# Performance work log

Hardware: AMD Instinct MI355X
Metric: run time of the kernel (lower is better)

Reference implementation:

```python
import jax, jax.numpy as jnp
import numpy as np

TEMPERATURE = 2.0


def _offdiag_idx(n):
    # flat indices of the off-diagonal entries of an [n, n] matrix, row-major,
    # reshaped to [n, n-1] (matches torch masked_select(~eye).view(n, n-1))
    idx = np.arange(n * n).reshape(n, n)
    return jnp.asarray(idx[~np.eye(n, dtype=bool)].reshape(n, n - 1))


def setup_inputs() -> dict:
    key = jax.random.key(0)
    k1, k2, k3, k4 = jax.random.split(key, 4)
    B, D = 256, 512
    return {
        "wt_emb": jax.random.normal(k1, (B, D), dtype=jnp.float32),
        "mt_emb": jax.random.normal(k2, (B, D), dtype=jnp.float32),
        "label_wt": jax.random.uniform(k3, (B,), dtype=jnp.float32),
        "label_mt": jax.random.uniform(k4, (B,), dtype=jnp.float32),
    }


def reference(wt_emb, mt_emb, label_wt, label_mt):
    t = TEMPERATURE
    features = jnp.concatenate([wt_emb, mt_emb], axis=0)            # [n, D]
    labels = jnp.concatenate([label_wt, label_mt], axis=0)[:, None]  # [n, 1]
    n = features.shape[0]

    # L1 label differences: [n, n]
    label_diffs = jnp.abs(labels[:, None, :] - labels[None, :, :]).sum(-1)

    # negative L2 feature distances (safe sqrt: diagonal is exactly 0)
    diff = features[:, None, :] - features[None, :, :]               # [n, n, D]
    sq = jnp.sum(diff * diff, axis=-1)                               # [n, n]
    dist = jnp.where(sq > 0, jnp.sqrt(jnp.where(sq > 0, sq, 1.0)), 0.0)
    logits = -dist / t
    logits = logits - jax.lax.stop_gradient(jnp.max(logits, axis=1, keepdims=True))
    exp_logits = jnp.exp(logits)

    # drop diagonal -> [n, n-1]
    off = _offdiag_idx(n)
    lo = logits.reshape(-1)[off]
    eo = exp_logits.reshape(-1)[off]
    ldo = label_diffs.reshape(-1)[off]

    # vectorized over positive index k: mask[i, k, j] = ld[i, j] >= ld[i, k]
    neg_mask = ldo[:, None, :] >= ldo[:, :, None]                    # [n, n-1, n-1]
    denom = jnp.sum(jnp.where(neg_mask, eo[:, None, :], 0.0), axis=-1)  # [n, n-1]
    pos_log_probs = lo - jnp.log(denom)                              # [n, n-1]
    return -jnp.sum(pos_log_probs) / (n * (n - 1))
```

## Files before the change

### kernel.cpp

```cpp
#include <hip/hip_runtime.h>


#define N 512
#define B 256
#define D 512
#define NT 512
#define NBLK (N / 2)

#define WS_SL    0
#define WS_NORM  512
#define WS_PART  1024
#define WS_FH    2048

typedef _Float16 half4_t  __attribute__((ext_vector_type(4)));
typedef _Float16 half8_t  __attribute__((ext_vector_type(8)));
typedef float    f32x4    __attribute__((ext_vector_type(4)));

__global__ __launch_bounds__(NT) void sort_rows_kernel(
    const float* __restrict__ wt, const float* __restrict__ mt,
    const float* __restrict__ lwt, const float* __restrict__ lmt,
    float* __restrict__ ws)
{
    const int t = threadIdx.x, b = blockIdx.x;
    __shared__ float slab[N];
    __shared__ int scnt[4];
    __shared__ float swred[NT / 64];
    slab[t] = (t < B) ? lwt[t] : lmt[t - B];
    if (t < 4) scnt[t] = 0;
    __syncthreads();

    const int jj = t >> 7, j = b * 4 + jj;
    const int c = t & 127;
    const float lj = slab[j];
    int r = 0;
    #pragma unroll
    for (int x = c * 4; x < c * 4 + 4; ++x) {
        const float v = slab[x];
        r += (v < lj || (v == lj && x < j)) ? 1 : 0;
    }
    #pragma unroll
    for (int off = 32; off > 0; off >>= 1)
        r += __shfl_down(r, off, 64);
    if ((t & 63) == 0) atomicAdd(&scnt[jj], r);
    __syncthreads();

    if (t < 4)
        ws[WS_SL + scnt[t]] = slab[b * 4 + t];

    const int rr = scnt[jj];
    const float* F = (j < B) ? (wt + (size_t)j * D) : (mt + (size_t)(j - B) * D);
    const float4 v = ((const float4*)F)[c];
    half4_t h;
    h[0] = (_Float16)v.x; h[1] = (_Float16)v.y;
    h[2] = (_Float16)v.z; h[3] = (_Float16)v.w;
    ((half4_t*)((_Float16*)(ws + WS_FH) + (size_t)rr * D))[c] = h;
    const float f0 = (float)h[0], f1 = (float)h[1];
    const float f2 = (float)h[2], f3 = (float)h[3];
    float nacc = f0 * f0 + f1 * f1 + f2 * f2 + f3 * f3;
    #pragma unroll
    for (int off = 32; off > 0; off >>= 1)
        nacc += __shfl_down(nacc, off, 64);
    if ((t & 63) == 0) swred[t >> 6] = nacc;
    __syncthreads();
    if (t < 4)
        ws[WS_NORM + scnt[t]] = swred[2 * t] + swred[2 * t + 1];
}

__global__ __launch_bounds__(NT) void rnc_main(float* __restrict__ ws)
{
    const int b = blockIdx.x, i0 = 2 * b, i1 = 2 * b + 1;
    const int t = threadIdx.x;
    const int w = t >> 6, lane = t & 63;

    __shared__ float sl[N];
    __shared__ float snm[N];
    __shared__ __align__(16) float sp0[N];
    __shared__ __align__(16) float sf0[N];
    __shared__ __align__(16) float sp1[N];
    __shared__ __align__(16) float sf1[N];
    __shared__ float sg0[N];
    __shared__ float sg1[N];
    __shared__ float sred[NT / 64];

    sl[t]  = ws[WS_SL + t];
    snm[t] = ws[WS_NORM + t];

    const _Float16* Fh = (const _Float16*)(ws + WS_FH);
    const int quad = lane >> 4, m = lane & 15;
    const _Float16* Ap = Fh + (size_t)(i0 + (m & 1)) * D + quad * 8;
    const _Float16* Bp[4];
    #pragma unroll
    for (int u = 0; u < 4; ++u)
        Bp[u] = Fh + (size_t)((w * 4 + u) * 16 + m) * D + quad * 8;

    f32x4 acc[4] = {{0.f,0.f,0.f,0.f},{0.f,0.f,0.f,0.f},
                    {0.f,0.f,0.f,0.f},{0.f,0.f,0.f,0.f}};
    #pragma unroll
    for (int k0 = 0; k0 < D; k0 += 32) {
        const half8_t a = *(const half8_t*)(Ap + k0);
        #pragma unroll
        for (int u = 0; u < 4; ++u) {
            const half8_t bb = *(const half8_t*)(Bp[u] + k0);
            acc[u] = __builtin_amdgcn_mfma_f32_16x16x32_f16(a, bb, acc[u], 0, 0, 0);
        }
    }
    if (quad == 0) {
        #pragma unroll
        for (int u = 0; u < 4; ++u) {
            const int col = w * 64 + u * 16 + m;
            sg0[col] = acc[u][0];
            sg1[col] = acc[u][1];
        }
    }
    __syncthreads();

    const float li0 = sl[i0], li1 = sl[i1];
    const float ni0 = snm[i0], ni1 = snm[i1];

    const float g0 = sg0[t];
    const float g1 = sg1[t];
    const float d0 = fmaxf(ni0 + snm[t] - 2.f * g0, 0.f);
    const float d1 = fmaxf(ni1 + snm[t] - 2.f * g1, 0.f);
    const float lg0 = -0.5f * sqrtf(d0);
    const float lg1 = -0.5f * sqrtf(d1);
    float lg_acc = 0.f;
    if (t != i0) lg_acc += lg0;
    if (t != i1) lg_acc += lg1;
    const float e0 = (t == i0) ? 0.f : __expf(lg0);
    const float e1 = (t == i1) ? 0.f : __expf(lg1);
    sp0[t] = e0; sf0[t] = e0;
    sp1[t] = e1; sf1[t] = e1;
    __syncthreads();

    if (w < 4) {
        float* arr = (w == 0) ? sp0 : (w == 1) ? sf0 : (w == 2) ? sp1 : sf1;
        float4* a4 = (float4*)arr;
        float4 u0 = a4[lane * 2], u1 = a4[lane * 2 + 1];
        float v0 = u0.x, v1 = u0.y, v2 = u0.z, v3 = u0.w;
        float v4 = u1.x, v5 = u1.y, v6 = u1.z, v7 = u1.w;
        if ((w & 1) == 0) {
            v1 += v0; v2 += v1; v3 += v2; v4 += v3; v5 += v4; v6 += v5; v7 += v6;
            float x = v7;
            #pragma unroll
            for (int off = 1; off < 64; off <<= 1) {
                const float y = __shfl_up(x, off, 64);
                if (lane >= off) x += y;
            }
            float ex = __shfl_up(x, 1, 64);
            if (lane == 0) ex = 0.f;
            v0 += ex; v1 += ex; v2 += ex; v3 += ex; v4 += ex; v5 += ex; v6 += ex; v7 += ex;
        } else {
            v6 += v7; v5 += v6; v4 += v5; v3 += v4; v2 += v3; v1 += v2; v0 += v1;
            float x = v0;
            #pragma unroll
            for (int off = 1; off < 64; off <<= 1) {
                const float y = __shfl_down(x, off, 64);
                if (lane + off < 64) x += y;
            }
            float ex = __shfl_down(x, 1, 64);
            if (lane == 63) ex = 0.f;
            v0 += ex; v1 += ex; v2 += ex; v3 += ex; v4 += ex; v5 += ex; v6 += ex; v7 += ex;
        }
        a4[lane * 2]     = make_float4(v0, v1, v2, v3);
        a4[lane * 2 + 1] = make_float4(v4, v5, v6, v7);
    }
    __syncthreads();

    float local = lg_acc;
    #pragma unroll
    for (int p = 0; p < 2; ++p) {
        const int x = t;
        const int ri = p ? i1 : i0;
        const float li = p ? li1 : li0;
        const float* SP = p ? sp1 : sp0;
        const float* SF = p ? sf1 : sf0;
        if (x != ri) {
            const float th = fabsf(li - sl[x]);
            int lo = 0, hi = ri + 1;
            while (lo < hi) {
                const int mid = (lo + hi) >> 1;
                if (fabsf(li - sl[mid]) >= th) lo = mid + 1; else hi = mid;
            }
            const int a = lo;
            lo = ri + 1; hi = N;
            while (lo < hi) {
                const int mid = (lo + hi) >> 1;
                if (fabsf(li - sl[mid]) >= th) hi = mid; else lo = mid + 1;
            }
            const int bb = lo;
            const float denom = ((a > 0) ? SP[a - 1] : 0.f) + ((bb < N) ? SF[bb] : 0.f);
            local -= __logf(denom);
        }
    }

    #pragma unroll
    for (int off = 32; off > 0; off >>= 1)
        local += __shfl_down(local, off, 64);
    if (lane == 0) sred[w] = local;
    __syncthreads();
    if (t == 0) {
        float sum = 0.f;
        #pragma unroll
        for (int k = 0; k < NT / 64; ++k) sum += sred[k];
        ws[WS_PART + b] = sum;
    }
}

__global__ __launch_bounds__(NBLK) void rnc_finalize(
    const float* __restrict__ ws, float* __restrict__ out)
{
    const int t = threadIdx.x;
    __shared__ float sred[NBLK / 64];
    float v = ws[WS_PART + t];
    #pragma unroll
    for (int off = 32; off > 0; off >>= 1)
        v += __shfl_down(v, off, 64);
    if ((t & 63) == 0) sred[t >> 6] = v;
    __syncthreads();
    if (t == 0) {
        float sum = 0.f;
        #pragma unroll
        for (int k = 0; k < NBLK / 64; ++k) sum += sred[k];
        out[0] = -sum / (float)((long)N * (N - 1));
    }
}

extern "C" void kernel_launch(void* const* d_in, const int* in_sizes, int n_in,
                              void* d_out, int out_size, void* d_ws, size_t ws_size,
                              hipStream_t stream) {
    const float* wt  = (const float*)d_in[0];
    const float* mt  = (const float*)d_in[1];
    const float* lwt = (const float*)d_in[2];
    const float* lmt = (const float*)d_in[3];
    float* out = (float*)d_out;
    float* ws  = (float*)d_ws;

    sort_rows_kernel<<<128, NT, 0, stream>>>(wt, mt, lwt, lmt, ws);
    rnc_main<<<NBLK, NT, 0, stream>>>(ws);
    rnc_finalize<<<1, NBLK, 0, stream>>>(ws, out);
}
```

Baseline: 83.37 us.

## Compute full Gram matrix in a separate MFMA kernel instead of per-block

Moves the feature Gram computation out of the per-row-pair main kernel into a dedicated kernel that computes the full 512x512 matrix with 32x32 MFMA tiles per wave and writes it to workspace. The main kernel now just loads its two Gram rows. This removes the heavy redundancy where every block streamed the full fp16 feature matrix and issued MFMAs using only two output rows per tile. It adds an extra kernel launch and a round trip of the Gram matrix through global memory.

```diff
diff --git a/kernel.cpp b/kernel.cpp
--- a/kernel.cpp
+++ b/kernel.cpp
@@ -11,6 +11,7 @@
 #define WS_NORM  512
 #define WS_PART  1024
 #define WS_FH    2048
+#define WS_G     (2048 + (N * D) / 2)
 
 typedef _Float16 half4_t  __attribute__((ext_vector_type(4)));
 typedef _Float16 half8_t  __attribute__((ext_vector_type(8)));
@@ -66,6 +67,46 @@
         ws[WS_NORM + scnt[t]] = swred[2 * t] + swred[2 * t + 1];
 }
 
+__global__ __launch_bounds__(256) void gram_kernel(float* __restrict__ ws)
+{
+    const int lane = threadIdx.x & 63;
+    const int wid  = blockIdx.x * 4 + (threadIdx.x >> 6);
+    const int ti = wid >> 4, tj = wid & 15;
+    const int quad = lane >> 4, m = lane & 15;
+
+    const _Float16* Fh = (const _Float16*)(ws + WS_FH);
+    const _Float16* A0 = Fh + (size_t)(ti * 32 + m) * D + quad * 8;
+    const _Float16* A1 = A0 + (size_t)16 * D;
+    const _Float16* B0 = Fh + (size_t)(tj * 32 + m) * D + quad * 8;
+    const _Float16* B1 = B0 + (size_t)16 * D;
+
+    f32x4 acc00 = {0.f, 0.f, 0.f, 0.f};
+    f32x4 acc01 = {0.f, 0.f, 0.f, 0.f};
+    f32x4 acc10 = {0.f, 0.f, 0.f, 0.f};
+    f32x4 acc11 = {0.f, 0.f, 0.f, 0.f};
+    #pragma unroll
+    for (int k0 = 0; k0 < D; k0 += 32) {
+        const half8_t a0 = *(const half8_t*)(A0 + k0);
+        const half8_t a1 = *(const half8_t*)(A1 + k0);
+        const half8_t b0 = *(const half8_t*)(B0 + k0);
+        const half8_t b1 = *(const half8_t*)(B1 + k0);
+        acc00 = __builtin_amdgcn_mfma_f32_16x16x32_f16(a0, b0, acc00, 0, 0, 0);
+        acc01 = __builtin_amdgcn_mfma_f32_16x16x32_f16(a0, b1, acc01, 0, 0, 0);
+        acc10 = __builtin_amdgcn_mfma_f32_16x16x32_f16(a1, b0, acc10, 0, 0, 0);
+        acc11 = __builtin_amdgcn_mfma_f32_16x16x32_f16(a1, b1, acc11, 0, 0, 0);
+    }
+    float* G = ws + WS_G;
+    const int r0 = ti * 32 + quad * 4;
+    const int c0 = tj * 32 + m;
+    #pragma unroll
+    for (int rg = 0; rg < 4; ++rg) {
+        G[(size_t)(r0 + rg) * N + c0]           = acc00[rg];
+        G[(size_t)(r0 + rg) * N + c0 + 16]      = acc01[rg];
+        G[(size_t)(r0 + 16 + rg) * N + c0]      = acc10[rg];
+        G[(size_t)(r0 + 16 + rg) * N + c0 + 16] = acc11[rg];
+    }
+}
+
 __global__ __launch_bounds__(NT) void rnc_main(float* __restrict__ ws)
 {
     const int b = blockIdx.x, i0 = 2 * b, i1 = 2 * b + 1;
@@ -78,47 +119,17 @@
     __shared__ __align__(16) float sf0[N];
     __shared__ __align__(16) float sp1[N];
     __shared__ __align__(16) float sf1[N];
-    __shared__ float sg0[N];
-    __shared__ float sg1[N];
     __shared__ float sred[NT / 64];
 
     sl[t]  = ws[WS_SL + t];
     snm[t] = ws[WS_NORM + t];
-
-    const _Float16* Fh = (const _Float16*)(ws + WS_FH);
-    const int quad = lane >> 4, m = lane & 15;
-    const _Float16* Ap = Fh + (size_t)(i0 + (m & 1)) * D + quad * 8;
-    const _Float16* Bp[4];
-    #pragma unroll
-    for (int u = 0; u < 4; ++u)
-        Bp[u] = Fh + (size_t)((w * 4 + u) * 16 + m) * D + quad * 8;
-
-    f32x4 acc[4] = {{0.f,0.f,0.f,0.f},{0.f,0.f,0.f,0.f},
-                    {0.f,0.f,0.f,0.f},{0.f,0.f,0.f,0.f}};
-    #pragma unroll
-    for (int k0 = 0; k0 < D; k0 += 32) {
-        const half8_t a = *(const half8_t*)(Ap + k0);
-        #pragma unroll
-        for (int u = 0; u < 4; ++u) {
-            const half8_t bb = *(const half8_t*)(Bp[u] + k0);
-            acc[u] = __builtin_amdgcn_mfma_f32_16x16x32_f16(a, bb, acc[u], 0, 0, 0);
-        }
-    }
-    if (quad == 0) {
-        #pragma unroll
-        for (int u = 0; u < 4; ++u) {
-            const int col = w * 64 + u * 16 + m;
-            sg0[col] = acc[u][0];
-            sg1[col] = acc[u][1];
-        }
-    }
-    __syncthreads();
-
+    __syncthreads();
     const float li0 = sl[i0], li1 = sl[i1];
     const float ni0 = snm[i0], ni1 = snm[i1];
 
-    const float g0 = sg0[t];
-    const float g1 = sg1[t];
+    const float* G = ws + WS_G;
+    const float g0 = G[(size_t)i0 * N + t];
+    const float g1 = G[(size_t)i1 * N + t];
     const float d0 = fmaxf(ni0 + snm[t] - 2.f * g0, 0.f);
     const float d1 = fmaxf(ni1 + snm[t] - 2.f * g1, 0.f);
     const float lg0 = -0.5f * sqrtf(d0);
@@ -236,6 +247,7 @@
     float* ws  = (float*)d_ws;
 
     sort_rows_kernel<<<128, NT, 0, stream>>>(wt, mt, lwt, lmt, ws);
+    gram_kernel<<<64, 256, 0, stream>>>(ws);
     rnc_main<<<NBLK, NT, 0, stream>>>(ws);
     rnc_finalize<<<1, NBLK, 0, stream>>>(ws, out);
 }
```

Result: faster. 76.15 us (-8.7%).
